# Kernel optimization log

Hardware: AMD Instinct MI355X
Metric: run time of the kernel (lower is better)

Reference implementation:

```python
import jax, jax.numpy as jnp
import numpy as np

N = 50000   # full-order mesh size
n = 10      # latent dim
MU = 32     # neighbourhood / window size
B = 8       # batch of snapshots


def setup_inputs() -> dict:
    key = jax.random.key(0)
    ks = jax.random.split(key, 6)
    x = jax.random.normal(ks[0], (B, N), jnp.float32)
    enc_w = jax.random.normal(ks[1], (n, N), jnp.float32) * 0.01  # torch Linear weight [n, N]
    enc_b = jax.random.normal(ks[2], (n,), jnp.float32) * 0.01
    decoder = jax.random.uniform(ks[3], (n, N), jnp.float32, minval=-0.01, maxval=0.01)
    bandwidth_layers = jax.random.uniform(ks[4], (n, n, N), jnp.float32, minval=-0.01, maxval=0.01)
    neighbours = jax.random.randint(ks[5], (N, MU), 0, N, jnp.int32)
    return dict(x=x, enc_w=enc_w, enc_b=enc_b, decoder=decoder,
                bandwidth_layers=bandwidth_layers, neighbours=neighbours)


def reference(x, enc_w, enc_b, decoder, bandwidth_layers, neighbours):
    mu = neighbours.shape[1]
    # encode: torch Linear -> x @ W.T + b                      [B, n]
    encoded = x @ enc_w.T + enc_b
    # bandwidths: bmm(encoded.repeat(n,1,1), bw).permute(1,0,2) -> sigmoid   [B, n, N]
    w = jax.nn.sigmoid(jnp.einsum('bk,ikp->bip', encoded, bandwidth_layers))
    # bubble window per scalar w: relu(1 - x^2/(w*mu)^2), normalized over mu  [B, n, N, mu]
    xs2 = (jnp.arange(mu, dtype=x.dtype) ** 2)  # [mu]
    win = jax.nn.relu(1.0 - xs2 / (w[..., None] * mu) ** 2)
    win = win / jnp.sum(win, axis=-1, keepdims=True)
    # gather decoder rows at each node's neighbours            [n, N, mu]
    gathered = jnp.take(decoder, neighbours, axis=1)
    # smooth_vec: sum over neighbourhood                       [B, n, N]
    smoothed = jnp.einsum('ipm,bipm->bip', gathered, win)
    # final bmm: encoded [B,1,n] @ smoothed [B,n,N] -> [B,N]
    return jnp.einsum('bi,bip->bp', encoded, smoothed)
```

## Files before the change

### kernel.cpp

```cpp
#include <hip/hip_runtime.h>
#include <hip/hip_bf16.h>

#define N_NODES 50000
#define NLAT 10
#define MU 32
#define BATCH 8
#define CHUNK 2000
#define NCHUNK 25
#define DT_STRIDE 16

__global__ __launch_bounds__(256) void encode_stage_a(
    const float* __restrict__ x, const float* __restrict__ enc_w,
    float* __restrict__ partial) {
    const int blk = blockIdx.x;
    const int c  = blk % NCHUNK;
    const int bi = blk / NCHUNK;
    const int b = bi / NLAT, i = bi % NLAT;
    const float4* xr = (const float4*)(x + (size_t)b * N_NODES + c * CHUNK);
    const float4* wr = (const float4*)(enc_w + (size_t)i * N_NODES + c * CHUNK);
    float part = 0.0f;
    for (int q = threadIdx.x; q < CHUNK / 4; q += 256) {
        float4 xv = xr[q], wv = wr[q];
        part += xv.x * wv.x + xv.y * wv.y + xv.z * wv.z + xv.w * wv.w;
    }
    for (int off = 32; off; off >>= 1) part += __shfl_down(part, off, 64);
    __shared__ float s[4];
    if ((threadIdx.x & 63) == 0) s[threadIdx.x >> 6] = part;
    __syncthreads();
    if (threadIdx.x == 0) partial[blk] = (s[0] + s[1]) + (s[2] + s[3]);
}

__global__ __launch_bounds__(128) void encode_stage_b(
    const float* __restrict__ partial, const float* __restrict__ enc_b,
    float* __restrict__ enc) {
    const int t = threadIdx.x;
    if (t < BATCH * NLAT) {
        float s = 0.0f;
        #pragma unroll
        for (int c = 0; c < NCHUNK; ++c) s += partial[t * NCHUNK + c];
        enc[t] = s + enc_b[t % NLAT];
    }
}

__global__ __launch_bounds__(256) void transpose_dec(
    const float* __restrict__ dec, float* __restrict__ dec_t) {
    const int p = blockIdx.x * 256 + threadIdx.x;
    if (p >= N_NODES) return;
    float v[DT_STRIDE];
    #pragma unroll
    for (int i = 0; i < NLAT; ++i) v[i] = dec[(size_t)i * N_NODES + p];
    #pragma unroll
    for (int i = NLAT; i < DT_STRIDE; ++i) v[i] = 0.0f;
    float4* dst = (float4*)(dec_t + (size_t)p * DT_STRIDE);
    #pragma unroll
    for (int q = 0; q < 4; ++q)
        dst[q] = make_float4(v[4*q], v[4*q+1], v[4*q+2], v[4*q+3]);
}

template<bool TR>
__global__ __launch_bounds__(256) void nrbs_main_kernel(
    const float* __restrict__ dec,
    const float* __restrict__ dec_t,
    const float* __restrict__ bw,
    const int*   __restrict__ nbr,
    const float* __restrict__ enc,
    float*       __restrict__ out) {
    __shared__ float s_enc[BATCH * NLAT];
    const int tid = threadIdx.x;
    if (tid < BATCH * NLAT) s_enc[tid] = enc[tid];
    __syncthreads();

    const int b  = tid & 7;
    const int nl = tid >> 3;
    const int p  = blockIdx.x * 32 + nl;
    if (p >= N_NODES) return;

    float inv[NLAT];
    float tmax = 0.0f;
    #pragma unroll
    for (int i = 0; i < NLAT; ++i) {
        float z = 0.0f;
        #pragma unroll
        for (int k = 0; k < NLAT; ++k)
            z = fmaf(s_enc[b * NLAT + k],
                     bw[((size_t)(i * NLAT + k)) * N_NODES + p], z);
        const float w = 1.0f / (1.0f + __expf(-z));
        const float t = w * (float)MU;
        tmax = fmaxf(tmax, t);
        inv[i] = 1.0f / (t * t);
    }
    const int mcap = min(MU, (int)tmax + 1);

    float asum[NLAT], ssum[NLAT];
    #pragma unroll
    for (int i = 0; i < NLAT; ++i) { asum[i] = 0.0f; ssum[i] = 0.0f; }

    const int4* nb4 = (const int4*)(nbr + (size_t)p * MU);
    for (int q = 0; 4 * q < mcap; ++q) {
        const int4 v = nb4[q];
        const int idx[4] = {v.x, v.y, v.z, v.w};
        #pragma unroll
        for (int j = 0; j < 4; ++j) {
            const int m = 4 * q + j;
            const float m2 = (float)(m * m);
            float g[NLAT];
            if (TR) {
                const float4* gp = (const float4*)(dec_t + (size_t)idx[j] * DT_STRIDE);
                const float4 g0 = gp[0], g1 = gp[1], g2 = gp[2];
                g[0]=g0.x; g[1]=g0.y; g[2]=g0.z; g[3]=g0.w;
                g[4]=g1.x; g[5]=g1.y; g[6]=g1.z; g[7]=g1.w;
                g[8]=g2.x; g[9]=g2.y;
            } else {
                #pragma unroll
                for (int i = 0; i < NLAT; ++i)
                    g[i] = dec[(size_t)i * N_NODES + idx[j]];
            }
            #pragma unroll
            for (int i = 0; i < NLAT; ++i) {
                const float win = fmaxf(0.0f, fmaf(-m2, inv[i], 1.0f));
                ssum[i] += win;
                asum[i] = fmaf(g[i], win, asum[i]);
            }
        }
    }

    float acc = 0.0f;
    #pragma unroll
    for (int i = 0; i < NLAT; ++i)
        acc = fmaf(s_enc[b * NLAT + i], asum[i] / ssum[i], acc);
    out[(size_t)b * N_NODES + p] = acc;
}

extern "C" void kernel_launch(void* const* d_in, const int* in_sizes, int n_in,
                              void* d_out, int out_size, void* d_ws, size_t ws_size,
                              hipStream_t stream) {
    const float* x       = (const float*)d_in[0];
    const float* enc_w   = (const float*)d_in[1];
    const float* enc_b   = (const float*)d_in[2];
    const float* decoder = (const float*)d_in[3];
    const float* bwl     = (const float*)d_in[4];
    const int*   nbr     = (const int*)d_in[5];
    float* out = (float*)d_out;

    float* enc     = (float*)d_ws;
    float* partial = (float*)((char*)d_ws + 1024);
    float* dec_t   = (float*)((char*)d_ws + 65536);
    const size_t need = 65536 + (size_t)N_NODES * DT_STRIDE * 4;

    encode_stage_a<<<BATCH * NLAT * NCHUNK, 256, 0, stream>>>(x, enc_w, partial);
    encode_stage_b<<<1, 128, 0, stream>>>(partial, enc_b, enc);

    const int blocks = (N_NODES + 31) / 32;
    if (ws_size >= need) {
        transpose_dec<<<(N_NODES + 255) / 256, 256, 0, stream>>>(decoder, dec_t);
        nrbs_main_kernel<true><<<blocks, 256, 0, stream>>>(
            decoder, dec_t, bwl, nbr, enc, out);
    } else {
        nrbs_main_kernel<false><<<blocks, 256, 0, stream>>>(
            decoder, dec_t, bwl, nbr, enc, out);
    }
}
```

Measured before the change: 111.7 us.

## Stage gathered decoder rows in LDS shared across batch lanes; fuse encode with transpose

The main kernel now cooperatively gathers each node's neighbour decoder rows into shared memory once per node. The eight batch threads split the neighbour loads and then all read from LDS, replacing eight redundant global gathers per node. The window cap is reduced with a max across the batch lanes so all share one loop bound, which may add iterations for some lanes. The encode partial-sum kernel and the decoder transpose are merged into one launch to drop a kernel launch, and the fallback path without workspace is removed. The added ~50KB LDS per block limits occupancy.

```diff
diff --git a/kernel.cpp b/kernel.cpp
--- a/kernel.cpp
+++ b/kernel.cpp
@@ -7,27 +7,46 @@
 #define BATCH 8
 #define CHUNK 2000
 #define NCHUNK 25
+#define ENC_BLOCKS (BATCH * NLAT * NCHUNK)
+#define TR_BLOCKS ((N_NODES + 255) / 256)
 #define DT_STRIDE 16
+#define NPB 32
+#define SG_MSTRIDE 388
 
-__global__ __launch_bounds__(256) void encode_stage_a(
+__global__ __launch_bounds__(256) void encode_a_transpose(
     const float* __restrict__ x, const float* __restrict__ enc_w,
-    float* __restrict__ partial) {
-    const int blk = blockIdx.x;
-    const int c  = blk % NCHUNK;
-    const int bi = blk / NCHUNK;
-    const int b = bi / NLAT, i = bi % NLAT;
-    const float4* xr = (const float4*)(x + (size_t)b * N_NODES + c * CHUNK);
-    const float4* wr = (const float4*)(enc_w + (size_t)i * N_NODES + c * CHUNK);
-    float part = 0.0f;
-    for (int q = threadIdx.x; q < CHUNK / 4; q += 256) {
-        float4 xv = xr[q], wv = wr[q];
-        part += xv.x * wv.x + xv.y * wv.y + xv.z * wv.z + xv.w * wv.w;
+    const float* __restrict__ dec,
+    float* __restrict__ partial, float* __restrict__ dec_t) {
+    const int bid = blockIdx.x;
+    if (bid < ENC_BLOCKS) {
+        const int c  = bid % NCHUNK;
+        const int bi = bid / NCHUNK;
+        const int b = bi / NLAT, i = bi % NLAT;
+        const float4* xr = (const float4*)(x + (size_t)b * N_NODES + c * CHUNK);
+        const float4* wr = (const float4*)(enc_w + (size_t)i * N_NODES + c * CHUNK);
+        float part = 0.0f;
+        for (int q = threadIdx.x; q < CHUNK / 4; q += 256) {
+            float4 xv = xr[q], wv = wr[q];
+            part += xv.x * wv.x + xv.y * wv.y + xv.z * wv.z + xv.w * wv.w;
+        }
+        for (int off = 32; off; off >>= 1) part += __shfl_down(part, off, 64);
+        __shared__ float s[4];
+        if ((threadIdx.x & 63) == 0) s[threadIdx.x >> 6] = part;
+        __syncthreads();
+        if (threadIdx.x == 0) partial[bid] = (s[0] + s[1]) + (s[2] + s[3]);
+    } else {
+        const int p = (bid - ENC_BLOCKS) * 256 + threadIdx.x;
+        if (p >= N_NODES) return;
+        float v[DT_STRIDE];
+        #pragma unroll
+        for (int i = 0; i < NLAT; ++i) v[i] = dec[(size_t)i * N_NODES + p];
+        #pragma unroll
+        for (int i = NLAT; i < DT_STRIDE; ++i) v[i] = 0.0f;
+        float4* dst = (float4*)(dec_t + (size_t)p * DT_STRIDE);
+        #pragma unroll
+        for (int q = 0; q < 4; ++q)
+            dst[q] = make_float4(v[4*q], v[4*q+1], v[4*q+2], v[4*q+3]);
     }
-    for (int off = 32; off; off >>= 1) part += __shfl_down(part, off, 64);
-    __shared__ float s[4];
-    if ((threadIdx.x & 63) == 0) s[threadIdx.x >> 6] = part;
-    __syncthreads();
-    if (threadIdx.x == 0) partial[blk] = (s[0] + s[1]) + (s[2] + s[3]);
 }
 
 __global__ __launch_bounds__(128) void encode_stage_b(
@@ -42,85 +61,80 @@
     }
 }
 
-__global__ __launch_bounds__(256) void transpose_dec(
-    const float* __restrict__ dec, float* __restrict__ dec_t) {
-    const int p = blockIdx.x * 256 + threadIdx.x;
-    if (p >= N_NODES) return;
-    float v[DT_STRIDE];
-    #pragma unroll
-    for (int i = 0; i < NLAT; ++i) v[i] = dec[(size_t)i * N_NODES + p];
-    #pragma unroll
-    for (int i = NLAT; i < DT_STRIDE; ++i) v[i] = 0.0f;
-    float4* dst = (float4*)(dec_t + (size_t)p * DT_STRIDE);
-    #pragma unroll
-    for (int q = 0; q < 4; ++q)
-        dst[q] = make_float4(v[4*q], v[4*q+1], v[4*q+2], v[4*q+3]);
-}
-
-template<bool TR>
 __global__ __launch_bounds__(256) void nrbs_main_kernel(
-    const float* __restrict__ dec,
     const float* __restrict__ dec_t,
     const float* __restrict__ bw,
     const int*   __restrict__ nbr,
     const float* __restrict__ enc,
     float*       __restrict__ out) {
     __shared__ float s_enc[BATCH * NLAT];
+    __shared__ float s_g[MU * SG_MSTRIDE];
     const int tid = threadIdx.x;
     if (tid < BATCH * NLAT) s_enc[tid] = enc[tid];
     __syncthreads();
 
     const int b  = tid & 7;
     const int nl = tid >> 3;
-    const int p  = blockIdx.x * 32 + nl;
-    if (p >= N_NODES) return;
+    const int p  = blockIdx.x * NPB + nl;
+    const bool act = (p < N_NODES);
 
     float inv[NLAT];
     float tmax = 0.0f;
-    #pragma unroll
-    for (int i = 0; i < NLAT; ++i) {
-        float z = 0.0f;
+    if (act) {
+        const float* bwp = bw + p;
         #pragma unroll
-        for (int k = 0; k < NLAT; ++k)
-            z = fmaf(s_enc[b * NLAT + k],
-                     bw[((size_t)(i * NLAT + k)) * N_NODES + p], z);
-        const float w = 1.0f / (1.0f + __expf(-z));
-        const float t = w * (float)MU;
-        tmax = fmaxf(tmax, t);
-        inv[i] = 1.0f / (t * t);
+        for (int i = 0; i < NLAT; ++i) {
+            float z = 0.0f;
+            #pragma unroll
+            for (int k = 0; k < NLAT; ++k)
+                z = fmaf(s_enc[b * NLAT + k],
+                         bwp[(size_t)(i * NLAT + k) * N_NODES], z);
+            const float w = 1.0f / (1.0f + __expf(-z));
+            const float t = w * (float)MU;
+            tmax = fmaxf(tmax, t);
+            inv[i] = 1.0f / (t * t);
+        }
     }
-    const int mcap = min(MU, (int)tmax + 1);
+    float tm = tmax;
+    tm = fmaxf(tm, __shfl_xor(tm, 1, 64));
+    tm = fmaxf(tm, __shfl_xor(tm, 2, 64));
+    tm = fmaxf(tm, __shfl_xor(tm, 4, 64));
+    const int mcap = min(MU, (int)tm + 1);
+
+    if (act) {
+        #pragma unroll
+        for (int j = 0; j < 4; ++j) {
+            const int m = b + 8 * j;
+            if (m < mcap) {
+                const int idx = nbr[(size_t)p * MU + m];
+                const float4* gp = (const float4*)(dec_t + (size_t)idx * DT_STRIDE);
+                const float4 g0 = gp[0], g1 = gp[1], g2 = gp[2];
+                float4* dst = (float4*)(s_g + m * SG_MSTRIDE + nl * 12);
+                dst[0] = g0; dst[1] = g1; dst[2] = g2;
+            }
+        }
+    }
+    __syncthreads();
+
+    if (!act) return;
 
     float asum[NLAT], ssum[NLAT];
     #pragma unroll
     for (int i = 0; i < NLAT; ++i) { asum[i] = 0.0f; ssum[i] = 0.0f; }
 
-    const int4* nb4 = (const int4*)(nbr + (size_t)p * MU);
-    for (int q = 0; 4 * q < mcap; ++q) {
-        const int4 v = nb4[q];
-        const int idx[4] = {v.x, v.y, v.z, v.w};
+    for (int m = 0; m < mcap; ++m) {
+        const float m2 = (float)(m * m);
+        const float* gr = s_g + m * SG_MSTRIDE + nl * 12;
+        const float4 ga = *(const float4*)(gr);
+        const float4 gb = *(const float4*)(gr + 4);
+        const float2 gc = *(const float2*)(gr + 8);
+        const float g[NLAT] = {ga.x, ga.y, ga.z, ga.w,
+                               gb.x, gb.y, gb.z, gb.w, gc.x, gc.y};
         #pragma unroll
-        for (int j = 0; j < 4; ++j) {
-            const int m = 4 * q + j;
-            const float m2 = (float)(m * m);
-            float g[NLAT];
-            if (TR) {
-                const float4* gp = (const float4*)(dec_t + (size_t)idx[j] * DT_STRIDE);
-                const float4 g0 = gp[0], g1 = gp[1], g2 = gp[2];
-                g[0]=g0.x; g[1]=g0.y; g[2]=g0.z; g[3]=g0.w;
-                g[4]=g1.x; g[5]=g1.y; g[6]=g1.z; g[7]=g1.w;
-                g[8]=g2.x; g[9]=g2.y;
-            } else {
-                #pragma unroll
-                for (int i = 0; i < NLAT; ++i)
-                    g[i] = dec[(size_t)i * N_NODES + idx[j]];
-            }
-            #pragma unroll
-            for (int i = 0; i < NLAT; ++i) {
-                const float win = fmaxf(0.0f, fmaf(-m2, inv[i], 1.0f));
-                ssum[i] += win;
-                asum[i] = fmaf(g[i], win, asum[i]);
-            }
+        for (int i = 0; i < NLAT; ++i) {
+            const float win = fmaxf(0.0f, fmaf(-m2, inv[i], 1.0f));
+            ssum[i] += win;
+            asum[i] = fmaf(g[i], win, asum[i]);
         }
     }
 
@@ -145,18 +159,11 @@
     float* enc     = (float*)d_ws;
     float* partial = (float*)((char*)d_ws + 1024);
     float* dec_t   = (float*)((char*)d_ws + 65536);
-    const size_t need = 65536 + (size_t)N_NODES * DT_STRIDE * 4;
 
-    encode_stage_a<<<BATCH * NLAT * NCHUNK, 256, 0, stream>>>(x, enc_w, partial);
+    encode_a_transpose<<<ENC_BLOCKS + TR_BLOCKS, 256, 0, stream>>>(
+        x, enc_w, decoder, partial, dec_t);
     encode_stage_b<<<1, 128, 0, stream>>>(partial, enc_b, enc);
 
-    const int blocks = (N_NODES + 31) / 32;
-    if (ws_size >= need) {
-        transpose_dec<<<(N_NODES + 255) / 256, 256, 0, stream>>>(decoder, dec_t);
-        nrbs_main_kernel<true><<<blocks, 256, 0, stream>>>(
-            decoder, dec_t, bwl, nbr, enc, out);
-    } else {
-        nrbs_main_kernel<false><<<blocks, 256, 0, stream>>>(
-            decoder, dec_t, bwl, nbr, enc, out);
-    }
+    const int blocks = (N_NODES + NPB - 1) / NPB;
+    nrbs_main_kernel<<<blocks, 256, 0, stream>>>(dec_t, bwl, nbr, enc, out);
 }
```

New measurement: 113.9 us. 1.02x slower.
